# Performance work log

Hardware: AMD Instinct MI355X
Metric: run time of the kernel (lower is better)

The kernel has to match this reference:

```python
import jax, jax.numpy as jnp
import numpy as np

B, N, L, E = 4, 8, 2048, 16384
CH = [128, 256, 256, 256]
EPS = 1e-5
USE_MAX = True


def setup_inputs() -> dict:
    key = jax.random.key(0)
    ks = jax.random.split(key, 10)
    d = {}
    d["x"] = jax.random.normal(ks[0], (B, N, CH[0], L), jnp.float32)
    d["edge_index"] = jax.random.randint(ks[1], (2, E), 0, L, dtype=jnp.int32)
    wspecs = [("W1", CH[0], CH[1]), ("W2", CH[1], CH[2]), ("W3", CH[2], CH[3]),
              ("W1s", CH[0], CH[1]), ("W2s", CH[1], CH[2]), ("W3s", CH[2], CH[3])]
    for i, (nm, ci, co) in enumerate(wspecs):
        std = (2.0 / (ci + co)) ** 0.5  # xavier_normal
        d[nm] = std * jax.random.normal(ks[2 + i], (ci, co), jnp.float32)
        d["b" + nm[1:]] = jnp.zeros((co,), jnp.float32)
    for nm, co in [("1", CH[1]), ("2", CH[2]), ("3", CH[3]),
                   ("1s", CH[1]), ("2s", CH[2]), ("3s", CH[3])]:
        d["g" + nm] = jnp.ones((co,), jnp.float32)
        d["be" + nm] = jnp.zeros((co,), jnp.float32)
    return d


def _gcn_norm(edge_index, num_nodes):
    # PyG gcn_norm with improved=True: A_hat = A + 2I, sym normalization.
    src, dst = edge_index[0], edge_index[1]
    loop = jnp.arange(num_nodes, dtype=src.dtype)
    src = jnp.concatenate([src, loop])
    dst = jnp.concatenate([dst, loop])
    w = jnp.concatenate([jnp.ones((edge_index.shape[1],), jnp.float32),
                         jnp.full((num_nodes,), 2.0, jnp.float32)])
    deg = jnp.zeros((num_nodes,), jnp.float32).at[dst].add(w)
    dis = jnp.where(deg > 0, jax.lax.rsqrt(deg), 0.0)
    return src, dst, dis[src] * w * dis[dst]


def _gcn(h, W, bias, src, dst, norm, num_nodes):
    # h: [G, L, Cin] node features for G independent copies of the shared graph
    hw = h @ W  # [G, L, Cout]
    msgs = hw[:, src, :] * norm[None, :, None]  # gather along nodes
    agg = jnp.zeros((h.shape[0], num_nodes, W.shape[1]), h.dtype).at[:, dst].add(msgs)
    return agg + bias


def _bn(x, g, be):
    # x: [Nb, C, L]; training-mode BatchNorm1d over (Nb, L) per channel
    m = x.mean(axis=(0, 2), keepdims=True)
    v = x.var(axis=(0, 2), keepdims=True)
    return g[None, :, None] * (x - m) * jax.lax.rsqrt(v + EPS) + be[None, :, None]


def _forward(x, edge_index, params):
    b, n, c, l = x.shape
    src, dst, norm = _gcn_norm(edge_index, l)
    xo = None
    for (W, bias, Ws, bs, g, be, gs, bes) in params:
        # per-element branch
        h = x.reshape(b * n, x.shape[2], l).transpose(0, 2, 1)  # [b*n, L, C]
        x1 = _gcn(h, W, bias, src, dst, norm, l).transpose(0, 2, 1)  # [b*n, Cout, L]
        x1 = _bn(x1, g, be)
        # symmetric pooled branch
        xp = jnp.max(x, axis=1) if USE_MAX else jnp.sum(x, axis=1)  # [b, C, L]
        x2 = _gcn(xp.transpose(0, 2, 1), Ws, bs, src, dst, norm, l).transpose(0, 2, 1)
        x2 = _bn(x2, gs, bes)
        co = x2.shape[1]
        x2 = jnp.broadcast_to(x2[:, None], (b, n, co, l)).reshape(b * n, co, l)
        xo = jax.nn.relu(x1 + x2)  # [b*n, Cout, L]
        x = xo.reshape(b, n, co, l)
    return xo  # final output is [b*n, CH[3], L] (not reshaped back)


def reference(x, edge_index, W1, b1, W2, b2, W3, b3, W1s, b1s, W2s, b2s, W3s, b3s,
              g1, be1, g2, be2, g3, be3, g1s, be1s, g2s, be2s, g3s, be3s):
    params = [(W1, b1, W1s, b1s, g1, be1, g1s, be1s),
              (W2, b2, W2s, b2s, g2, be2, g2s, be2s),
              (W3, b3, W3s, b3s, g3, be3, g3s, be3s)]
    return _forward(x, edge_index, params)
```

## Files before the change

### kernel.cpp

```cpp
#include <hip/hip_runtime.h>
#include <math.h>

#define LNODES 2048
#define NEDGE 16384
#define GBIG 32
#define GSM 4
#define NCOUT 256
#define BN_EPS 1e-5f
#define ND 32

typedef unsigned short u16;
typedef __attribute__((ext_vector_type(8))) short bf16x8;
typedef __attribute__((ext_vector_type(4))) float f32x4;

__device__ __forceinline__ unsigned pk2(float a, float b) {
  unsigned ua = __float_as_uint(a); ua += 0x7fffu + ((ua >> 16) & 1u);
  unsigned ub = __float_as_uint(b); ub += 0x7fffu + ((ub >> 16) & 1u);
  return (ua >> 16) | (ub & 0xffff0000u);
}
__device__ __forceinline__ float blo(unsigned u) { return __uint_as_float(u << 16); }
__device__ __forceinline__ float bhi(unsigned u) { return __uint_as_float(u & 0xffff0000u); }

__device__ __forceinline__ void gl16(const u16* g, u16* l) {
  __builtin_amdgcn_global_load_lds(
      (const __attribute__((address_space(1))) void*)g,
      (__attribute__((address_space(3))) void*)l, 16, 0, 0);
}


struct WCvt {
  const float* src[6];
  u16* dst[6];
  int ci[6];
};

__global__ __launch_bounds__(256) void setup1_k(const int* __restrict__ ei,
                                                float* __restrict__ deg,
                                                int* __restrict__ cnt,
                                                WCvt wp,
                                                const float* __restrict__ x_in,
                                                u16* __restrict__ XT0) {
  __shared__ float T[64][65];
  const int bid = blockIdx.x;
  const int t = threadIdx.x;
  if (bid < 64) {
    int e = bid * 256 + t;
    int d = ei[NEDGE + e];
    atomicAdd(&deg[d], 1.0f);
    atomicAdd(&cnt[d], 1);
  } else if (bid < 160) {
    const int w = bid - 64;
    const int bz = w >> 4;
    const int Ci = wp.ci[bz];
    const int ci0 = ((w >> 2) & 3) * 64;
    if (ci0 >= Ci) return;
    const float* W = wp.src[bz];
    u16* WT = wp.dst[bz];
    const int co0 = (w & 3) * 64;
    const int tr = t >> 4;
    const int tc = (t & 15) * 4;
#pragma unroll
    for (int p = 0; p < 4; ++p) {
      int ci = ci0 + tr + p * 16;
      float4 v = *reinterpret_cast<const float4*>(&W[(size_t)ci * NCOUT + co0 + tc]);
      T[tr + p * 16][tc + 0] = v.x; T[tr + p * 16][tc + 1] = v.y;
      T[tr + p * 16][tc + 2] = v.z; T[tr + p * 16][tc + 3] = v.w;
    }
    __syncthreads();
    const int ci = ci0 + tc;
    const int kt = ci >> 5;
    const int kk = ci & 31;
#pragma unroll
    for (int p = 0; p < 4; ++p) {
      int co = co0 + tr + p * 16;
      uint2 o = {pk2(T[tc + 0][co - co0], T[tc + 1][co - co0]),
                 pk2(T[tc + 2][co - co0], T[tc + 3][co - co0])};
      size_t idx = (size_t)kt * 8192 + (unsigned)((co * 32 + kk) ^ ((co & 7) << 3));
      *reinterpret_cast<uint2*>(&WT[idx]) = o;
    }
  } else {
    const int w = bid - 160;
    const int g = w >> 6;
    const int n0 = (w & 31) * 64;
    const int c0 = ((w >> 5) & 1) * 64;
    const int tr = t >> 4;
    const int tc = (t & 15) * 4;
#pragma unroll
    for (int p = 0; p < 4; ++p) {
      int ci = c0 + tr + p * 16;
      float4 v = *reinterpret_cast<const float4*>(&x_in[((size_t)g * 128 + ci) * LNODES + n0 + tc]);
      T[tr + p * 16][tc + 0] = v.x; T[tr + p * 16][tc + 1] = v.y;
      T[tr + p * 16][tc + 2] = v.z; T[tr + p * 16][tc + 3] = v.w;
    }
    __syncthreads();
#pragma unroll
    for (int p = 0; p < 4; ++p) {
      int nd = tr + p * 16;
      uint2 o = {pk2(T[tc + 0][nd], T[tc + 1][nd]), pk2(T[tc + 2][nd], T[tc + 3][nd])};
      *reinterpret_cast<uint2*>(&XT0[((size_t)g * LNODES + n0 + nd) * 128 + c0 + tc]) = o;
    }
  }
}

__global__ __launch_bounds__(256) void setup2_k(const float* __restrict__ deg,
                                                float* __restrict__ dis,
                                                float* __restrict__ selfn,
                                                const int* __restrict__ cnt,
                                                int* __restrict__ rp) {
  __shared__ int part[256];
  const int t = threadIdx.x;
  if (blockIdx.x == 8) {
    int base = t * 8;
    int loc[8];
    int s = 0;
#pragma unroll
    for (int j = 0; j < 8; ++j) { loc[j] = s; s += cnt[base + j]; }
    part[t] = s;
    __syncthreads();
    for (int off = 1; off < 256; off <<= 1) {
      int v = (t >= off) ? part[t - off] : 0;
      __syncthreads();
      part[t] += v;
      __syncthreads();
    }
    int excl = (t == 0) ? 0 : part[t - 1];
#pragma unroll
    for (int j = 0; j < 8; ++j) rp[base + j] = excl + loc[j];
    if (t == 255) rp[LNODES] = part[255];
  } else {
    int i = blockIdx.x * 256 + t;
    float di = rsqrtf(deg[i] + 2.0f);
    dis[i] = di;
    selfn[i] = 2.0f * di * di;
  }
}

__global__ __launch_bounds__(256) void setup3_k(const int* __restrict__ ei,
                                                const int* __restrict__ rp,
                                                int* __restrict__ fillc,
                                                const float* __restrict__ dis,
                                                int* __restrict__ col,
                                                float* __restrict__ wn,
                                                const u16* __restrict__ X,
                                                u16* __restrict__ XP) {
  const int bid = blockIdx.x;
  const int t = threadIdx.x;
  if (bid < 64) {
    int e = bid * 256 + t;
    int s = ei[e], d = ei[NEDGE + e];
    int pos = rp[d] + atomicAdd(&fillc[d], 1);
    col[pos] = s;
    wn[pos] = dis[s] * dis[d];
  } else {
    const int per = 128 * LNODES;
    int i = (bid - 64) * 256 + t;
    size_t f = (size_t)i * 8;
    int b = (int)(f / per);
    size_t rem = f - (size_t)b * per;
    const u16* base = X + (size_t)b * 8 * per + rem;
    uint4 u = *reinterpret_cast<const uint4*>(base);
    float m0 = blo(u.x), m1 = bhi(u.x), m2 = blo(u.y), m3 = bhi(u.y);
    float m4 = blo(u.z), m5 = bhi(u.z), m6 = blo(u.w), m7 = bhi(u.w);
#pragma unroll
    for (int j = 1; j < 8; ++j) {
      uint4 v = *reinterpret_cast<const uint4*>(base + (size_t)j * per);
      m0 = fmaxf(m0, blo(v.x)); m1 = fmaxf(m1, bhi(v.x));
      m2 = fmaxf(m2, blo(v.y)); m3 = fmaxf(m3, bhi(v.y));
      m4 = fmaxf(m4, blo(v.z)); m5 = fmaxf(m5, bhi(v.z));
      m6 = fmaxf(m6, blo(v.w)); m7 = fmaxf(m7, bhi(v.w));
    }
    uint4 o = {pk2(m0, m1), pk2(m2, m3), pk2(m4, m5), pk2(m6, m7)};
    *reinterpret_cast<uint4*>(XP + (size_t)b * per + rem) = o;
  }
}

__device__ __forceinline__ void coef_ld(const float* __restrict__ st,
                                        const float* __restrict__ ga,
                                        const float* __restrict__ be,
                                        const float* __restrict__ gs,
                                        const float* __restrict__ bes,
                                        float* lk1, float* lk2, float* lcc, int t) {
  float sA = 0.f, qA = 0.f, sB = 0.f, qB = 0.f;
#pragma unroll
  for (int x = 0; x < 8; ++x) {
    sA += st[x * NCOUT + t];
    qA += st[2048 + x * NCOUT + t];
    sB += st[4096 + x * NCOUT + t];
    qB += st[6144 + x * NCOUT + t];
  }
  const float c1 = (float)(GBIG * LNODES), c2 = (float)(GSM * LNODES);
  float mA = sA / c1;
  float vA = qA / c1 - mA * mA;
  float kA = ga[t] * rsqrtf(vA + BN_EPS);
  float mB = sB / c2;
  float vB = qB / c2 - mB * mB;
  float kB = gs[t] * rsqrtf(vB + BN_EPS);
  lk1[t] = kA;
  lk2[t] = kB;
  lcc[t] = be[t] - kA * mA + bes[t] - kB * mB;
}

template <int MODE>
__global__ __launch_bounds__(256) void gemm3_k(const u16* __restrict__ B1,
                                               const u16* __restrict__ B2,
                                               const float* __restrict__ st,
                                               const float* __restrict__ ga,
                                               const float* __restrict__ be,
                                               const float* __restrict__ gs,
                                               const float* __restrict__ bes,
                                               const u16* __restrict__ WbT,
                                               const u16* __restrict__ WsT,
                                               u16* __restrict__ HW1,
                                               u16* __restrict__ hw2) {
  constexpr int Cin = (MODE == 0) ? 128 : 256;
  constexpr int BSH = 64 * Cin;
  constexpr int EPI = 64 * 264;
  constexpr int BASE = (BSH > EPI) ? BSH : EPI;
  __shared__ __align__(16) u16 smem[BASE + 8192];
  __shared__ float lk1[NCOUT], lk2[NCOUT], lcc[NCOUT];
  u16* Wsh = smem + BASE;
  const int z = blockIdx.z;
  const bool sym = z < GSM;
  const int g = sym ? z : z - GSM;
  u16* out = sym ? hw2 : HW1;
  const int n0 = blockIdx.x * 64;
  const int t = threadIdx.x;
  constexpr int OPR = Cin / 8;
  constexpr int RPI = 256 / OPR;
  constexpr int NIT = 64 / RPI;
  const int ro = t / OPR;
  const int ch8 = (t % OPR) * 8;

  float K1[8], K2[8], CC[8];
  if constexpr (MODE == 1) {
    coef_ld(st, ga, be, gs, bes, lk1, lk2, lcc, t);
    __syncthreads();
#pragma unroll
    for (int j = 0; j < 8; ++j) { K1[j] = lk1[ch8 + j]; K2[j] = lk2[ch8 + j]; CC[j] = lcc[ch8 + j]; }
  }

#define BIDX(r, c) ((((r) * Cin) + (c)) ^ (((r) & 7) << 3))

  if (MODE == 0 || sym) {
    if constexpr (MODE == 0) {
      const u16* src = (sym ? B2 : B1) + ((size_t)g * LNODES + n0) * Cin + ch8;
#pragma unroll
      for (int it = 0; it < NIT; ++it) {
        int row = it * RPI + ro;
        uint4 v = *reinterpret_cast<const uint4*>(&src[(size_t)row * Cin]);
        *reinterpret_cast<uint4*>(&smem[BIDX(row, ch8)]) = v;
      }
    } else {
      const size_t b2o = ((size_t)g * LNODES + n0) * NCOUT + ch8;
      const size_t a1b = ((size_t)(g * 8) * LNODES + n0) * NCOUT + ch8;
      const size_t nstep = (size_t)LNODES * NCOUT;
      for (int it = 0; it < NIT; ++it) {
        int row = it * RPI + ro;
        uint4 a2 = *reinterpret_cast<const uint4*>(&B2[b2o + (size_t)row * NCOUT]);
        float t0 = K2[0] * blo(a2.x) + CC[0], t1 = K2[1] * bhi(a2.x) + CC[1];
        float t2 = K2[2] * blo(a2.y) + CC[2], t3 = K2[3] * bhi(a2.y) + CC[3];
        float t4 = K2[4] * blo(a2.z) + CC[4], t5 = K2[5] * bhi(a2.z) + CC[5];
        float t6 = K2[6] * blo(a2.w) + CC[6], t7 = K2[7] * bhi(a2.w) + CC[7];
        float m0 = 0.f, m1 = 0.f, m2 = 0.f, m3 = 0.f, m4 = 0.f, m5 = 0.f, m6 = 0.f, m7 = 0.f;
#pragma unroll
        for (int n = 0; n < 8; ++n) {
          uint4 a1 = *reinterpret_cast<const uint4*>(&B1[a1b + n * nstep + (size_t)row * NCOUT]);
          m0 = fmaxf(m0, K1[0] * blo(a1.x) + t0); m1 = fmaxf(m1, K1[1] * bhi(a1.x) + t1);
          m2 = fmaxf(m2, K1[2] * blo(a1.y) + t2); m3 = fmaxf(m3, K1[3] * bhi(a1.y) + t3);
          m4 = fmaxf(m4, K1[4] * blo(a1.z) + t4); m5 = fmaxf(m5, K1[5] * bhi(a1.z) + t5);
          m6 = fmaxf(m6, K1[6] * blo(a1.w) + t6); m7 = fmaxf(m7, K1[7] * bhi(a1.w) + t7);
        }
        uint4 ov = {pk2(m0, m1), pk2(m2, m3), pk2(m4, m5), pk2(m6, m7)};
        *reinterpret_cast<uint4*>(&smem[BIDX(row, ch8)]) = ov;
      }
    }
  } else {
    const size_t b1o = ((size_t)g * LNODES + n0) * NCOUT + ch8;
    const size_t b2o = ((size_t)(g >> 3) * LNODES + n0) * NCOUT + ch8;
#pragma unroll
    for (int it = 0; it < NIT; ++it) {
      int row = it * RPI + ro;
      uint4 a1 = *reinterpret_cast<const uint4*>(&B1[b1o + (size_t)row * NCOUT]);
      uint4 a2 = *reinterpret_cast<const uint4*>(&B2[b2o + (size_t)row * NCOUT]);
      float o0 = fmaxf(K1[0] * blo(a1.x) + K2[0] * blo(a2.x) + CC[0], 0.f);
      float o1 = fmaxf(K1[1] * bhi(a1.x) + K2[1] * bhi(a2.x) + CC[1], 0.f);
      float o2 = fmaxf(K1[2] * blo(a1.y) + K2[2] * blo(a2.y) + CC[2], 0.f);
      float o3 = fmaxf(K1[3] * bhi(a1.y) + K2[3] * bhi(a2.y) + CC[3], 0.f);
      float o4 = fmaxf(K1[4] * blo(a1.z) + K2[4] * blo(a2.z) + CC[4], 0.f);
      float o5 = fmaxf(K1[5] * bhi(a1.z) + K2[5] * bhi(a2.z) + CC[5], 0.f);
      float o6 = fmaxf(K1[6] * blo(a1.w) + K2[6] * blo(a2.w) + CC[6], 0.f);
      float o7 = fmaxf(K1[7] * bhi(a1.w) + K2[7] * bhi(a2.w) + CC[7], 0.f);
      uint4 ov = {pk2(o0, o1), pk2(o2, o3), pk2(o4, o5), pk2(o6, o7)};
      *reinterpret_cast<uint4*>(&smem[BIDX(row, ch8)]) = ov;
    }
  }

  const int wv = t >> 6;
  const int lane = t & 63;
  const int q = lane >> 4, l = lane & 15;
  f32x4 zero = {0.f, 0.f, 0.f, 0.f};
  f32x4 acc[4][4];
#pragma unroll
  for (int i = 0; i < 4; ++i)
#pragma unroll
    for (int j = 0; j < 4; ++j) acc[i][j] = zero;

  const u16* Wmat = sym ? WsT : WbT;
#pragma unroll
  for (int kt = 0; kt < Cin / 32; ++kt) {
    __syncthreads();
    const u16* ws = Wmat + (size_t)kt * 8192;
#pragma unroll
    for (int c = 0; c < 4; ++c)
      gl16(ws + c * 2048 + t * 8, &Wsh[c * 2048 + t * 8]);
    __syncthreads();
    bf16x8 af[4], bx[4];
#pragma unroll
    for (int fi = 0; fi < 4; ++fi) {
      int row = wv * 64 + fi * 16 + l;
      af[fi] = *reinterpret_cast<const bf16x8*>(&Wsh[(row * 32 + q * 8) ^ ((row & 7) << 3)]);
    }
#pragma unroll
    for (int fj = 0; fj < 4; ++fj) {
      int brow = fj * 16 + l;
      bx[fj] = *reinterpret_cast<const bf16x8*>(&smem[BIDX(brow, kt * 32 + q * 8)]);
    }
#pragma unroll
    for (int fi = 0; fi < 4; ++fi)
#pragma unroll
      for (int fj = 0; fj < 4; ++fj)
        acc[fi][fj] = __builtin_amdgcn_mfma_f32_16x16x32_bf16(af[fi], bx[fj], acc[fi][fj], 0, 0, 0);
  }
#undef BIDX

  __syncthreads();
  u16* Csh = smem;
#pragma unroll
  for (int fi = 0; fi < 4; ++fi) {
#pragma unroll
    for (int fj = 0; fj < 4; ++fj) {
      int co_l = wv * 64 + fi * 16 + q * 4;
      int nd_l = fj * 16 + l;
      uint2 pkd = {pk2(acc[fi][fj][0], acc[fi][fj][1]),
                   pk2(acc[fi][fj][2], acc[fi][fj][3])};
      *reinterpret_cast<uint2*>(&Csh[nd_l * 264 + co_l]) = pkd;
    }
  }
  __syncthreads();
#pragma unroll
  for (int p = 0; p < 8; ++p) {
    int idx = p * 256 + t;
    int nd = idx >> 5;
    int c8 = (idx & 31) * 8;
    uint4 v = *reinterpret_cast<const uint4*>(&Csh[nd * 264 + c8]);
    *reinterpret_cast<uint4*>(&out[((size_t)g * LNODES + n0 + nd) * NCOUT + c8]) = v;
  }
}

__global__ __launch_bounds__(256) void agg_comb_k(const u16* __restrict__ HW1,
                                                  const u16* __restrict__ hw2,
                                                  const int* __restrict__ col,
                                                  const float* __restrict__ wn,
                                                  const int* __restrict__ rp,
                                                  const float* __restrict__ selfn,
                                                  u16* __restrict__ AGG1,
                                                  u16* __restrict__ agg2,
                                                  float* __restrict__ st) {
  __shared__ float lsum[8][NCOUT], lsq[8][NCOUT];
  const int bid = blockIdx.x;
  const int t = threadIdx.x;
  const int wv = t >> 6;
  float* sumO;
  float* sqO;
  int shard;
  if (bid < 1024) {
    int slot = bid >> 3;
    int chunk = slot & 63;
    int g0 = (bid & 7) + 8 * (slot >> 6);
    const int d0 = chunk * ND;
    const int h = (t >> 5) & 1;
    const int ch = (t & 31) * 8;
    const u16* baseh = HW1 + (size_t)(g0 + 16 * h) * LNODES * NCOUT;
    u16* outh = AGG1 + (size_t)(g0 + 16 * h) * LNODES * NCOUT;
    float s0 = 0.f, s1 = 0.f, s2 = 0.f, s3 = 0.f, s4 = 0.f, s5 = 0.f, s6 = 0.f, s7 = 0.f;
    float q0 = 0.f, q1 = 0.f, q2 = 0.f, q3 = 0.f, q4 = 0.f, q5 = 0.f, q6 = 0.f, q7 = 0.f;
    for (int i = wv; i < ND; i += 4) {
      int d = d0 + i;
      int e0 = rp[d], e1 = rp[d + 1];
      float sw = selfn[d];
      uint4 u = *reinterpret_cast<const uint4*>(&baseh[(size_t)d * NCOUT + ch]);
      float a0 = sw * blo(u.x), a1 = sw * bhi(u.x), a2 = sw * blo(u.y), a3 = sw * bhi(u.y);
      float a4 = sw * blo(u.z), a5 = sw * bhi(u.z), a6 = sw * blo(u.w), a7 = sw * bhi(u.w);
      int e = e0;
      const int e4 = e0 + ((e1 - e0) & ~3);
      for (; e < e4; e += 4) {
        int i0 = col[e + 0], i1 = col[e + 1], i2 = col[e + 2], i3 = col[e + 3];
        float w0 = wn[e + 0], w1 = wn[e + 1], w2 = wn[e + 2], w3 = wn[e + 3];
        uint4 v0 = *reinterpret_cast<const uint4*>(&baseh[(size_t)i0 * NCOUT + ch]);
        uint4 v1 = *reinterpret_cast<const uint4*>(&baseh[(size_t)i1 * NCOUT + ch]);
        uint4 v2 = *reinterpret_cast<const uint4*>(&baseh[(size_t)i2 * NCOUT + ch]);
        uint4 v3 = *reinterpret_cast<const uint4*>(&baseh[(size_t)i3 * NCOUT + ch]);
        a0 += w0 * blo(v0.x); a1 += w0 * bhi(v0.x); a2 += w0 * blo(v0.y); a3 += w0 * bhi(v0.y);
        a4 += w0 * blo(v0.z); a5 += w0 * bhi(v0.z); a6 += w0 * blo(v0.w); a7 += w0 * bhi(v0.w);
        a0 += w1 * blo(v1.x); a1 += w1 * bhi(v1.x); a2 += w1 * blo(v1.y); a3 += w1 * bhi(v1.y);
        a4 += w1 * blo(v1.z); a5 += w1 * bhi(v1.z); a6 += w1 * blo(v1.w); a7 += w1 * bhi(v1.w);
        a0 += w2 * blo(v2.x); a1 += w2 * bhi(v2.x); a2 += w2 * blo(v2.y); a3 += w2 * bhi(v2.y);
        a4 += w2 * blo(v2.z); a5 += w2 * bhi(v2.z); a6 += w2 * blo(v2.w); a7 += w2 * bhi(v2.w);
        a0 += w3 * blo(v3.x); a1 += w3 * bhi(v3.x); a2 += w3 * blo(v3.y); a3 += w3 * bhi(v3.y);
        a4 += w3 * blo(v3.z); a5 += w3 * bhi(v3.z); a6 += w3 * blo(v3.w); a7 += w3 * bhi(v3.w);
      }
      for (; e < e1; ++e) {
        int ci = col[e];
        float w = wn[e];
        uint4 v = *reinterpret_cast<const uint4*>(&baseh[(size_t)ci * NCOUT + ch]);
        a0 += w * blo(v.x); a1 += w * bhi(v.x); a2 += w * blo(v.y); a3 += w * bhi(v.y);
        a4 += w * blo(v.z); a5 += w * bhi(v.z); a6 += w * blo(v.w); a7 += w * bhi(v.w);
      }
      uint4 o = {pk2(a0, a1), pk2(a2, a3), pk2(a4, a5), pk2(a6, a7)};
      *reinterpret_cast<uint4*>(&outh[(size_t)d * NCOUT + ch]) = o;
      s0 += a0; s1 += a1; s2 += a2; s3 += a3; s4 += a4; s5 += a5; s6 += a6; s7 += a7;
      q0 += a0 * a0; q1 += a1 * a1; q2 += a2 * a2; q3 += a3 * a3;
      q4 += a4 * a4; q5 += a5 * a5; q6 += a6 * a6; q7 += a7 * a7;
    }
    int row = wv * 2 + h;
    float4 sa = {s0, s1, s2, s3}, sb = {s4, s5, s6, s7};
    float4 qa = {q0, q1, q2, q3}, qb = {q4, q5, q6, q7};
    *reinterpret_cast<float4*>(&lsum[row][ch]) = sa;
    *reinterpret_cast<float4*>(&lsum[row][ch + 4]) = sb;
    *reinterpret_cast<float4*>(&lsq[row][ch]) = qa;
    *reinterpret_cast<float4*>(&lsq[row][ch + 4]) = qb;
    sumO = st; sqO = st + 2048; shard = (bid & 7) * NCOUT;
  } else {
    int b2 = bid - 1024;
    int g = b2 & (GSM - 1);
    int chunk = b2 >> 2;
    const int d0 = chunk * ND;
    const int lc = (t & 63) * 4;
    const u16* base = hw2 + (size_t)g * LNODES * NCOUT;
    float4 s = {0.f, 0.f, 0.f, 0.f}, qq = {0.f, 0.f, 0.f, 0.f};
    for (int i = wv; i < ND; i += 4) {
      int d = d0 + i;
      int e0 = rp[d], e1 = rp[d + 1];
      float sw = selfn[d];
      uint2 u = *reinterpret_cast<const uint2*>(&base[(size_t)d * NCOUT + lc]);
      float4 a = {sw * blo(u.x), sw * bhi(u.x), sw * blo(u.y), sw * bhi(u.y)};
      int e = e0;
      const int e4 = e0 + ((e1 - e0) & ~3);
      for (; e < e4; e += 4) {
        int i0 = col[e + 0], i1 = col[e + 1], i2 = col[e + 2], i3 = col[e + 3];
        float w0 = wn[e + 0], w1 = wn[e + 1], w2 = wn[e + 2], w3 = wn[e + 3];
        uint2 v0 = *reinterpret_cast<const uint2*>(&base[(size_t)i0 * NCOUT + lc]);
        uint2 v1 = *reinterpret_cast<const uint2*>(&base[(size_t)i1 * NCOUT + lc]);
        uint2 v2 = *reinterpret_cast<const uint2*>(&base[(size_t)i2 * NCOUT + lc]);
        uint2 v3 = *reinterpret_cast<const uint2*>(&base[(size_t)i3 * NCOUT + lc]);
        a.x += w0 * blo(v0.x); a.y += w0 * bhi(v0.x); a.z += w0 * blo(v0.y); a.w += w0 * bhi(v0.y);
        a.x += w1 * blo(v1.x); a.y += w1 * bhi(v1.x); a.z += w1 * blo(v1.y); a.w += w1 * bhi(v1.y);
        a.x += w2 * blo(v2.x); a.y += w2 * bhi(v2.x); a.z += w2 * blo(v2.y); a.w += w2 * bhi(v2.y);
        a.x += w3 * blo(v3.x); a.y += w3 * bhi(v3.x); a.z += w3 * blo(v3.y); a.w += w3 * bhi(v3.y);
      }
      for (; e < e1; ++e) {
        float w = wn[e];
        uint2 v = *reinterpret_cast<const uint2*>(&base[(size_t)col[e] * NCOUT + lc]);
        a.x += w * blo(v.x); a.y += w * bhi(v.x); a.z += w * blo(v.y); a.w += w * bhi(v.y);
      }
      uint2 o = {pk2(a.x, a.y), pk2(a.z, a.w)};
      *reinterpret_cast<uint2*>(&agg2[((size_t)g * LNODES + d) * NCOUT + lc]) = o;
      s.x += a.x; s.y += a.y; s.z += a.z; s.w += a.w;
      qq.x += a.x * a.x; qq.y += a.y * a.y; qq.z += a.z * a.z; qq.w += a.w * a.w;
    }
    *reinterpret_cast<float4*>(&lsum[wv][lc]) = s;
    *reinterpret_cast<float4*>(&lsq[wv][lc]) = qq;
    float4 z4 = {0.f, 0.f, 0.f, 0.f};
    *reinterpret_cast<float4*>(&lsum[wv + 4][lc]) = z4;
    *reinterpret_cast<float4*>(&lsq[wv + 4][lc]) = z4;
    sumO = st + 4096; sqO = st + 6144; shard = (b2 & 7) * NCOUT;
  }
  __syncthreads();
  float ts = 0.f, tq = 0.f;
#pragma unroll
  for (int r = 0; r < 8; ++r) {
    ts += lsum[r][t];
    tq += lsq[r][t];
  }
  atomicAdd(&sumO[shard + t], ts);
  atomicAdd(&sqO[shard + t], tq);
}

__global__ __launch_bounds__(256) void fuse_tr_bf_k(const u16* __restrict__ A1,
                                                    const u16* __restrict__ A2,
                                                    const float* __restrict__ st,
                                                    const float* __restrict__ ga,
                                                    const float* __restrict__ be,
                                                    const float* __restrict__ gs,
                                                    const float* __restrict__ bes,
                                                    float* __restrict__ O) {
  __shared__ float T[64][65];
  __shared__ float lk1[NCOUT], lk2[NCOUT], lcc[NCOUT];
  const int g = blockIdx.z;
  const int d0 = blockIdx.x * 64;
  const int c0 = blockIdx.y * 64;
  const int b = g >> 3;
  const int t = threadIdx.x;
  coef_ld(st, ga, be, gs, bes, lk1, lk2, lcc, t);
  __syncthreads();
  const int tr = t >> 4;
  const int tc = (t & 15) * 4;
#pragma unroll
  for (int p = 0; p < 4; ++p) {
    int d = d0 + tr + p * 16;
    uint2 a1 = *reinterpret_cast<const uint2*>(&A1[((size_t)g * LNODES + d) * NCOUT + c0 + tc]);
    uint2 a2 = *reinterpret_cast<const uint2*>(&A2[((size_t)b * LNODES + d) * NCOUT + c0 + tc]);
    int cb = c0 + tc;
    T[tr + p * 16][tc + 0] = fmaxf(lk1[cb+0] * blo(a1.x) + lk2[cb+0] * blo(a2.x) + lcc[cb+0], 0.f);
    T[tr + p * 16][tc + 1] = fmaxf(lk1[cb+1] * bhi(a1.x) + lk2[cb+1] * bhi(a2.x) + lcc[cb+1], 0.f);
    T[tr + p * 16][tc + 2] = fmaxf(lk1[cb+2] * blo(a1.y) + lk2[cb+2] * blo(a2.y) + lcc[cb+2], 0.f);
    T[tr + p * 16][tc + 3] = fmaxf(lk1[cb+3] * bhi(a1.y) + lk2[cb+3] * bhi(a2.y) + lcc[cb+3], 0.f);
  }
  __syncthreads();
#pragma unroll
  for (int p = 0; p < 4; ++p) {
    int c = tr + p * 16;
    float4 o = {T[tc + 0][c], T[tc + 1][c], T[tc + 2][c], T[tc + 3][c]};
    *reinterpret_cast<float4*>(&O[((size_t)g * NCOUT + c0 + c) * LNODES + d0 + tc]) = o;
  }
}


extern "C" void kernel_launch(void* const* d_in, const int* in_sizes, int n_in,
                              void* d_out, int out_size, void* d_ws, size_t ws_size,
                              hipStream_t stream) {
  const float* x_in = (const float*)d_in[0];
  const int* ei = (const int*)d_in[1];
  const float* W[3]   = {(const float*)d_in[2],  (const float*)d_in[4],  (const float*)d_in[6]};
  const float* Wsym[3]= {(const float*)d_in[8],  (const float*)d_in[10], (const float*)d_in[12]};
  const float* ga[3]  = {(const float*)d_in[14], (const float*)d_in[16], (const float*)d_in[18]};
  const float* be[3]  = {(const float*)d_in[15], (const float*)d_in[17], (const float*)d_in[19]};
  const float* gs[3]  = {(const float*)d_in[20], (const float*)d_in[22], (const float*)d_in[24]};
  const float* bes[3] = {(const float*)d_in[21], (const float*)d_in[23], (const float*)d_in[25]};

  const size_t EBIG = (size_t)GBIG * LNODES * NCOUT;
  const size_t ESM = (size_t)GSM * LNODES * NCOUT;
  char* p = (char*)d_ws;
  u16* XT0  = (u16*)p; p += (size_t)GBIG * LNODES * 128 * 2;
  u16* AGG1 = (u16*)p; p += EBIG * 2;
  u16* agg2 = (u16*)p; p += ESM * 2;
  u16* xp   = (u16*)p; p += ESM * 2;
  u16* hw2  = (u16*)p; p += ESM * 2;
  u16* WbT[3], *WsT[3];
  for (int i = 0; i < 3; ++i) { WbT[i] = (u16*)p; p += NCOUT * NCOUT * 2; }
  for (int i = 0; i < 3; ++i) { WsT[i] = (u16*)p; p += NCOUT * NCOUT * 2; }
  int*   rp   = (int*)p;   p += 2064 * 4;
  float* dis  = (float*)p; p += LNODES * 4;
  float* selfn= (float*)p; p += LNODES * 4;
  char* zbase = p;
  float* deg  = (float*)p; p += LNODES * 4;
  int*   cnt  = (int*)p;   p += LNODES * 4;
  int*   fillc= (int*)p;   p += LNODES * 4;
  int*   col  = (int*)p;   p += (NEDGE + 8) * 4;
  float* wn   = (float*)p; p += (NEDGE + 8) * 4;
  float* stats= (float*)p; p += 3 * 4 * 2048 * 4;
  size_t zsize = (size_t)(p - zbase);

  u16* HW1 = (u16*)d_out;
  float* stL[3] = {stats, stats + 8192, stats + 16384};

  hipMemsetAsync(zbase, 0, zsize, stream);
  WCvt wc;
  for (int i = 0; i < 3; ++i) {
    wc.src[i] = W[i];     wc.dst[i] = WbT[i];     wc.ci[i] = (i == 0) ? 128 : 256;
    wc.src[3 + i] = Wsym[i]; wc.dst[3 + i] = WsT[i]; wc.ci[3 + i] = (i == 0) ? 128 : 256;
  }
  setup1_k<<<2208, 256, 0, stream>>>(ei, deg, cnt, wc, x_in, XT0);
  setup2_k<<<9, 256, 0, stream>>>(deg, dis, selfn, cnt, rp);
  setup3_k<<<576, 256, 0, stream>>>(ei, rp, fillc, dis, col, wn, XT0, xp);

  dim3 ggrid(LNODES / 64, 1, GBIG + GSM);
  gemm3_k<0><<<ggrid, 256, 0, stream>>>(XT0, xp, nullptr, nullptr, nullptr, nullptr,
                                        nullptr, WbT[0], WsT[0], HW1, hw2);
  agg_comb_k<<<1280, 256, 0, stream>>>(HW1, hw2, col, wn, rp, selfn, AGG1, agg2, stL[0]);
  gemm3_k<1><<<ggrid, 256, 0, stream>>>(AGG1, agg2, stL[0], ga[0], be[0], gs[0], bes[0],
                                        WbT[1], WsT[1], HW1, hw2);
  agg_comb_k<<<1280, 256, 0, stream>>>(HW1, hw2, col, wn, rp, selfn, AGG1, agg2, stL[1]);
  gemm3_k<1><<<ggrid, 256, 0, stream>>>(AGG1, agg2, stL[1], ga[1], be[1], gs[1], bes[1],
                                        WbT[2], WsT[2], HW1, hw2);
  agg_comb_k<<<1280, 256, 0, stream>>>(HW1, hw2, col, wn, rp, selfn, AGG1, agg2, stL[2]);
  fuse_tr_bf_k<<<dim3(LNODES / 64, NCOUT / 64, GBIG), 256, 0, stream>>>(
      AGG1, agg2, stL[2], ga[2], be[2], gs[2], bes[2], (float*)d_out);
}
```

Baseline: 335.3 us.

## Fuse layer-0 max-pool into GEMM and prefetch next weight tile during MFMA

The max-pool over the set dimension for layer 0 moves out of setup3_k and into the symmetric-branch blocks of gemm3_k<0>. This removes the intermediate xp buffer and its write and re-read. The GEMM k-loop now issues the async LDS load of the next weight tile right after reading the current fragments, so weight loads overlap the MFMA work instead of sitting between barriers. The sym blocks in MODE 0 now read 8x the input, which may create load imbalance across blocks.

```diff
diff --git a/kernel.cpp b/kernel.cpp
--- a/kernel.cpp
+++ b/kernel.cpp
@@ -140,38 +140,12 @@
                                                 int* __restrict__ fillc,
                                                 const float* __restrict__ dis,
                                                 int* __restrict__ col,
-                                                float* __restrict__ wn,
-                                                const u16* __restrict__ X,
-                                                u16* __restrict__ XP) {
-  const int bid = blockIdx.x;
-  const int t = threadIdx.x;
-  if (bid < 64) {
-    int e = bid * 256 + t;
-    int s = ei[e], d = ei[NEDGE + e];
-    int pos = rp[d] + atomicAdd(&fillc[d], 1);
-    col[pos] = s;
-    wn[pos] = dis[s] * dis[d];
-  } else {
-    const int per = 128 * LNODES;
-    int i = (bid - 64) * 256 + t;
-    size_t f = (size_t)i * 8;
-    int b = (int)(f / per);
-    size_t rem = f - (size_t)b * per;
-    const u16* base = X + (size_t)b * 8 * per + rem;
-    uint4 u = *reinterpret_cast<const uint4*>(base);
-    float m0 = blo(u.x), m1 = bhi(u.x), m2 = blo(u.y), m3 = bhi(u.y);
-    float m4 = blo(u.z), m5 = bhi(u.z), m6 = blo(u.w), m7 = bhi(u.w);
-#pragma unroll
-    for (int j = 1; j < 8; ++j) {
-      uint4 v = *reinterpret_cast<const uint4*>(base + (size_t)j * per);
-      m0 = fmaxf(m0, blo(v.x)); m1 = fmaxf(m1, bhi(v.x));
-      m2 = fmaxf(m2, blo(v.y)); m3 = fmaxf(m3, bhi(v.y));
-      m4 = fmaxf(m4, blo(v.z)); m5 = fmaxf(m5, bhi(v.z));
-      m6 = fmaxf(m6, blo(v.w)); m7 = fmaxf(m7, bhi(v.w));
-    }
-    uint4 o = {pk2(m0, m1), pk2(m2, m3), pk2(m4, m5), pk2(m6, m7)};
-    *reinterpret_cast<uint4*>(XP + (size_t)b * per + rem) = o;
-  }
+                                                float* __restrict__ wn) {
+  int e = blockIdx.x * 256 + threadIdx.x;
+  int s = ei[e], d = ei[NEDGE + e];
+  int pos = rp[d] + atomicAdd(&fillc[d], 1);
+  col[pos] = s;
+  wn[pos] = dis[s] * dis[d];
 }
 
 __device__ __forceinline__ void coef_ld(const float* __restrict__ st,
@@ -213,6 +187,7 @@
                                                u16* __restrict__ HW1,
                                                u16* __restrict__ hw2) {
   constexpr int Cin = (MODE == 0) ? 128 : 256;
+  constexpr int NT = Cin / 32;
   constexpr int BSH = 64 * Cin;
   constexpr int EPI = 64 * 264;
   constexpr int BASE = (BSH > EPI) ? BSH : EPI;
@@ -225,6 +200,12 @@
   u16* out = sym ? hw2 : HW1;
   const int n0 = blockIdx.x * 64;
   const int t = threadIdx.x;
+  const u16* Wmat = sym ? WsT : WbT;
+
+#pragma unroll
+  for (int c = 0; c < 4; ++c)
+    gl16(Wmat + c * 2048 + t * 8, &Wsh[c * 2048 + t * 8]);
+
   constexpr int OPR = Cin / 8;
   constexpr int RPI = 256 / OPR;
   constexpr int NIT = 64 / RPI;
@@ -241,9 +222,9 @@
 
 #define BIDX(r, c) ((((r) * Cin) + (c)) ^ (((r) & 7) << 3))
 
-  if (MODE == 0 || sym) {
-    if constexpr (MODE == 0) {
-      const u16* src = (sym ? B2 : B1) + ((size_t)g * LNODES + n0) * Cin + ch8;
+  if constexpr (MODE == 0) {
+    if (!sym) {
+      const u16* src = B1 + ((size_t)g * LNODES + n0) * Cin + ch8;
 #pragma unroll
       for (int it = 0; it < NIT; ++it) {
         int row = it * RPI + ro;
@@ -251,30 +232,26 @@
         *reinterpret_cast<uint4*>(&smem[BIDX(row, ch8)]) = v;
       }
     } else {
-      const size_t b2o = ((size_t)g * LNODES + n0) * NCOUT + ch8;
-      const size_t a1b = ((size_t)(g * 8) * LNODES + n0) * NCOUT + ch8;
-      const size_t nstep = (size_t)LNODES * NCOUT;
+      const size_t a1b = ((size_t)(g * 8) * LNODES + n0) * Cin + ch8;
+      const size_t nstep = (size_t)LNODES * Cin;
       for (int it = 0; it < NIT; ++it) {
         int row = it * RPI + ro;
-        uint4 a2 = *reinterpret_cast<const uint4*>(&B2[b2o + (size_t)row * NCOUT]);
-        float t0 = K2[0] * blo(a2.x) + CC[0], t1 = K2[1] * bhi(a2.x) + CC[1];
-        float t2 = K2[2] * blo(a2.y) + CC[2], t3 = K2[3] * bhi(a2.y) + CC[3];
-        float t4 = K2[4] * blo(a2.z) + CC[4], t5 = K2[5] * bhi(a2.z) + CC[5];
-        float t6 = K2[6] * blo(a2.w) + CC[6], t7 = K2[7] * bhi(a2.w) + CC[7];
-        float m0 = 0.f, m1 = 0.f, m2 = 0.f, m3 = 0.f, m4 = 0.f, m5 = 0.f, m6 = 0.f, m7 = 0.f;
-#pragma unroll
-        for (int n = 0; n < 8; ++n) {
-          uint4 a1 = *reinterpret_cast<const uint4*>(&B1[a1b + n * nstep + (size_t)row * NCOUT]);
-          m0 = fmaxf(m0, K1[0] * blo(a1.x) + t0); m1 = fmaxf(m1, K1[1] * bhi(a1.x) + t1);
-          m2 = fmaxf(m2, K1[2] * blo(a1.y) + t2); m3 = fmaxf(m3, K1[3] * bhi(a1.y) + t3);
-          m4 = fmaxf(m4, K1[4] * blo(a1.z) + t4); m5 = fmaxf(m5, K1[5] * bhi(a1.z) + t5);
-          m6 = fmaxf(m6, K1[6] * blo(a1.w) + t6); m7 = fmaxf(m7, K1[7] * bhi(a1.w) + t7);
+        uint4 v = *reinterpret_cast<const uint4*>(&B1[a1b + (size_t)row * Cin]);
+        float m0 = blo(v.x), m1 = bhi(v.x), m2 = blo(v.y), m3 = bhi(v.y);
+        float m4 = blo(v.z), m5 = bhi(v.z), m6 = blo(v.w), m7 = bhi(v.w);
+#pragma unroll
+        for (int n = 1; n < 8; ++n) {
+          uint4 a = *reinterpret_cast<const uint4*>(&B1[a1b + n * nstep + (size_t)row * Cin]);
+          m0 = fmaxf(m0, blo(a.x)); m1 = fmaxf(m1, bhi(a.x));
+          m2 = fmaxf(m2, blo(a.y)); m3 = fmaxf(m3, bhi(a.y));
+          m4 = fmaxf(m4, blo(a.z)); m5 = fmaxf(m5, bhi(a.z));
+          m6 = fmaxf(m6, blo(a.w)); m7 = fmaxf(m7, bhi(a.w));
         }
         uint4 ov = {pk2(m0, m1), pk2(m2, m3), pk2(m4, m5), pk2(m6, m7)};
         *reinterpret_cast<uint4*>(&smem[BIDX(row, ch8)]) = ov;
       }
     }
-  } else {
+  } else if (!sym) {
     const size_t b1o = ((size_t)g * LNODES + n0) * NCOUT + ch8;
     const size_t b2o = ((size_t)(g >> 3) * LNODES + n0) * NCOUT + ch8;
 #pragma unroll
@@ -293,6 +270,29 @@
       uint4 ov = {pk2(o0, o1), pk2(o2, o3), pk2(o4, o5), pk2(o6, o7)};
       *reinterpret_cast<uint4*>(&smem[BIDX(row, ch8)]) = ov;
     }
+  } else {
+    const size_t b2o = ((size_t)g * LNODES + n0) * NCOUT + ch8;
+    const size_t a1b = ((size_t)(g * 8) * LNODES + n0) * NCOUT + ch8;
+    const size_t nstep = (size_t)LNODES * NCOUT;
+    for (int it = 0; it < NIT; ++it) {
+      int row = it * RPI + ro;
+      uint4 a2 = *reinterpret_cast<const uint4*>(&B2[b2o + (size_t)row * NCOUT]);
+      float t0 = K2[0] * blo(a2.x) + CC[0], t1 = K2[1] * bhi(a2.x) + CC[1];
+      float t2 = K2[2] * blo(a2.y) + CC[2], t3 = K2[3] * bhi(a2.y) + CC[3];
+      float t4 = K2[4] * blo(a2.z) + CC[4], t5 = K2[5] * bhi(a2.z) + CC[5];
+      float t6 = K2[6] * blo(a2.w) + CC[6], t7 = K2[7] * bhi(a2.w) + CC[7];
+      float m0 = 0.f, m1 = 0.f, m2 = 0.f, m3 = 0.f, m4 = 0.f, m5 = 0.f, m6 = 0.f, m7 = 0.f;
+#pragma unroll
+      for (int n = 0; n < 8; ++n) {
+        uint4 a1 = *reinterpret_cast<const uint4*>(&B1[a1b + n * nstep + (size_t)row * NCOUT]);
+        m0 = fmaxf(m0, K1[0] * blo(a1.x) + t0); m1 = fmaxf(m1, K1[1] * bhi(a1.x) + t1);
+        m2 = fmaxf(m2, K1[2] * blo(a1.y) + t2); m3 = fmaxf(m3, K1[3] * bhi(a1.y) + t3);
+        m4 = fmaxf(m4, K1[4] * blo(a1.z) + t4); m5 = fmaxf(m5, K1[5] * bhi(a1.z) + t5);
+        m6 = fmaxf(m6, K1[6] * blo(a1.w) + t6); m7 = fmaxf(m7, K1[7] * bhi(a1.w) + t7);
+      }
+      uint4 ov = {pk2(m0, m1), pk2(m2, m3), pk2(m4, m5), pk2(m6, m7)};
+      *reinterpret_cast<uint4*>(&smem[BIDX(row, ch8)]) = ov;
+    }
   }
 
   const int wv = t >> 6;
@@ -305,14 +305,8 @@
 #pragma unroll
     for (int j = 0; j < 4; ++j) acc[i][j] = zero;
 
-  const u16* Wmat = sym ? WsT : WbT;
-#pragma unroll
-  for (int kt = 0; kt < Cin / 32; ++kt) {
-    __syncthreads();
-    const u16* ws = Wmat + (size_t)kt * 8192;
-#pragma unroll
-    for (int c = 0; c < 4; ++c)
-      gl16(ws + c * 2048 + t * 8, &Wsh[c * 2048 + t * 8]);
+#pragma unroll
+  for (int kt = 0; kt < NT; ++kt) {
     __syncthreads();
     bf16x8 af[4], bx[4];
 #pragma unroll
@@ -324,6 +318,13 @@
     for (int fj = 0; fj < 4; ++fj) {
       int brow = fj * 16 + l;
       bx[fj] = *reinterpret_cast<const bf16x8*>(&smem[BIDX(brow, kt * 32 + q * 8)]);
+    }
+    __syncthreads();
+    if (kt + 1 < NT) {
+      const u16* ws = Wmat + (size_t)(kt + 1) * 8192;
+#pragma unroll
+      for (int c = 0; c < 4; ++c)
+        gl16(ws + c * 2048 + t * 8, &Wsh[c * 2048 + t * 8]);
     }
 #pragma unroll
     for (int fi = 0; fi < 4; ++fi)
@@ -544,7 +545,6 @@
   u16* XT0  = (u16*)p; p += (size_t)GBIG * LNODES * 128 * 2;
   u16* AGG1 = (u16*)p; p += EBIG * 2;
   u16* agg2 = (u16*)p; p += ESM * 2;
-  u16* xp   = (u16*)p; p += ESM * 2;
   u16* hw2  = (u16*)p; p += ESM * 2;
   u16* WbT[3], *WsT[3];
   for (int i = 0; i < 3; ++i) { WbT[i] = (u16*)p; p += NCOUT * NCOUT * 2; }
@@ -572,10 +572,10 @@
   }
   setup1_k<<<2208, 256, 0, stream>>>(ei, deg, cnt, wc, x_in, XT0);
   setup2_k<<<9, 256, 0, stream>>>(deg, dis, selfn, cnt, rp);
-  setup3_k<<<576, 256, 0, stream>>>(ei, rp, fillc, dis, col, wn, XT0, xp);
+  setup3_k<<<64, 256, 0, stream>>>(ei, rp, fillc, dis, col, wn);
 
   dim3 ggrid(LNODES / 64, 1, GBIG + GSM);
-  gemm3_k<0><<<ggrid, 256, 0, stream>>>(XT0, xp, nullptr, nullptr, nullptr, nullptr,
+  gemm3_k<0><<<ggrid, 256, 0, stream>>>(XT0, nullptr, nullptr, nullptr, nullptr, nullptr,
                                         nullptr, WbT[0], WsT[0], HW1, hw2);
   agg_comb_k<<<1280, 256, 0, stream>>>(HW1, hw2, col, wn, rp, selfn, AGG1, agg2, stL[0]);
   gemm3_k<1><<<ggrid, 256, 0, stream>>>(AGG1, agg2, stL[0], ga[0], be[0], gs[0], bes[0],
```

Result: no change. 333.6 us, median of 4 (-0.5%).
